# Kernel optimization log

Measured on AMD Instinct MI355X. Metric: run time of the kernel, lower is better.

The kernel has to match this reference:

```python
import jax, jax.numpy as jnp
import numpy as np

N_NODES = 100000
N_EDGES = 1600000
IN_DIM = 128
HID = 64
OUT_DIM = 3


def _glorot(key, shape):
    fan_in, fan_out = shape[0], shape[1]
    std = (2.0 / (fan_in + fan_out)) ** 0.5
    return jax.random.normal(key, shape, jnp.float32) * std


def setup_inputs() -> dict:
    key = jax.random.key(0)
    ks = jax.random.split(key, 12)
    x = jax.random.normal(ks[0], (N_NODES, IN_DIM), jnp.float32)
    edge_index = jax.random.randint(ks[1], (2, N_EDGES), 0, N_NODES, dtype=jnp.int32)
    return {
        "x": x,
        "edge_index": edge_index,
        "W1": _glorot(ks[2], (IN_DIM, HID)), "b1": jnp.zeros((HID,), jnp.float32),
        "W2": _glorot(ks[3], (HID, HID)), "b2": jnp.zeros((HID,), jnp.float32),
        "W3": _glorot(ks[4], (HID, HID)), "b3": jnp.zeros((HID,), jnp.float32),
        "W4": _glorot(ks[5], (HID, HID // 2)), "b4": jnp.zeros((HID // 2,), jnp.float32),
        "Wh": _glorot(ks[6], (HID // 2, OUT_DIM)), "bh": jnp.zeros((OUT_DIM,), jnp.float32),
    }


def reference(x, edge_index, W1, b1, W2, b2, W3, b3, W4, b4, Wh, bh):
    n = x.shape[0]
    self_loops = jnp.arange(n, dtype=edge_index.dtype)
    src = jnp.concatenate([edge_index[0], self_loops])  # message sources j
    dst = jnp.concatenate([edge_index[1], self_loops])  # aggregation targets i
    # symmetric GCN normalization with self-loops: deg over targets (unit edge weights)
    deg = jax.ops.segment_sum(jnp.ones_like(dst, jnp.float32), dst, num_segments=n)
    dinv = jnp.where(deg > 0, jax.lax.rsqrt(deg), 0.0)
    norm = dinv[src] * dinv[dst]  # [E+N]

    def gcn(h, W, b):
        h = h @ W  # transform first (PyG GCNConv order)
        agg = jax.ops.segment_sum(h[src] * norm[:, None], dst, num_segments=n)
        return agg + b

    h = jax.nn.relu(gcn(x, W1, b1))   # dropout is identity in eval mode
    h = jax.nn.relu(gcn(h, W2, b2))
    h = jax.nn.relu(gcn(h, W3, b3))
    h = jax.nn.relu(gcn(h, W4, b4))
    return h @ Wh + bh  # [N, 3]
```

## Files before the change

### kernel.cpp

```cpp
#include <hip/hip_runtime.h>
#include <hip/hip_bf16.h>
#include <hip/hip_fp16.h>
#include <cstdint>


#define MAXD 512
#define EB   8192

__global__ __launch_bounds__(256) void hist1_k(const int* __restrict__ ei,
                                               int* __restrict__ histM,
                                               int E, int ND) {
    __shared__ int hist[MAXD];
    const int tid = threadIdx.x, b = blockIdx.x;
    hist[tid] = 0; hist[tid + 256] = 0;
    __syncthreads();
    const int base = b * EB;
#pragma unroll 2
    for (int it = 0; it < EB / 256; it += 4) {
        int d[4]; bool ok[4];
#pragma unroll
        for (int u = 0; u < 4; ++u) {
            int e = base + (it + u) * 256 + tid;
            ok[u] = e < E;
            d[u] = ok[u] ? ei[E + e] : 0;
        }
#pragma unroll
        for (int u = 0; u < 4; ++u)
            if (ok[u]) atomicAdd(&hist[d[u] >> 8], 1);
    }
    __syncthreads();
    histM[(size_t)b * MAXD + tid] = hist[tid];
    histM[(size_t)b * MAXD + tid + 256] = hist[tid + 256];
}

__global__ __launch_bounds__(256) void scan_digits_k(int* __restrict__ histM,
                                                     int* __restrict__ totals,
                                                     int NBLK) {
    __shared__ int s[256];
    const int t = threadIdx.x, dg = blockIdx.x;
    int v = (t < NBLK) ? histM[(size_t)t * MAXD + dg] : 0;
    s[t] = v;
    __syncthreads();
    for (int off = 1; off < 256; off <<= 1) {
        int x = (t >= off) ? s[t - off] : 0;
        __syncthreads();
        s[t] += x;
        __syncthreads();
    }
    if (t < NBLK) histM[(size_t)t * MAXD + dg] = s[t] - v;
    if (t == 255) totals[dg] = s[255];
}

__global__ __launch_bounds__(512) void scan_base_k(const int* __restrict__ totals,
                                                   int* __restrict__ cb, int ND) {
    __shared__ int s[512];
    const int t = threadIdx.x;
    int v = (t < ND) ? totals[t] : 0;
    s[t] = v;
    __syncthreads();
    for (int off = 1; off < 512; off <<= 1) {
        int x = (t >= off) ? s[t - off] : 0;
        __syncthreads();
        s[t] += x;
        __syncthreads();
    }
    if (t < ND) cb[t] = s[t] - v;
    if (t == 511) cb[ND] = s[511];
}

template <int K, int OUT, bool HALF_OUT>
__device__ __forceinline__ void gemm_body(const float* __restrict__ H,
                                          const float* __restrict__ W,
                                          const float* __restrict__ dinv,
                                          void* __restrict__ Tout, int n, int bx) {
    constexpr int TX  = OUT / 4;
    constexpr int TY  = 256 / TX;
    constexpr int BM  = TY * 4;
    constexpr int BK  = 32;
    constexpr int PAD = 4;

    __shared__ float At[BK][BM + PAD];
    __shared__ float Ws[BK][OUT];

    const int t    = threadIdx.x;
    const int cx   = t % TX;
    const int ry   = t / TX;
    const int row0 = bx * BM;

    float acc[4][4] = {{0.f}};
    const int arow = t >> 3;
    const int af4  = t & 7;

    for (int k0 = 0; k0 < K; k0 += BK) {
#pragma unroll
        for (int p = 0; p < BM / 32; ++p) {
            int r  = arow + p * 32;
            int gr = row0 + r;
            int grc = gr < n ? gr : n - 1;
            float4 v = *reinterpret_cast<const float4*>(
                H + (size_t)grc * K + k0 + af4 * 4);
            At[af4 * 4 + 0][r] = v.x;
            At[af4 * 4 + 1][r] = v.y;
            At[af4 * 4 + 2][r] = v.z;
            At[af4 * 4 + 3][r] = v.w;
        }
#pragma unroll
        for (int p = 0; p < (BK * OUT) / 1024; ++p) {
            int idx = t + p * 256;
            int wk  = idx / (OUT / 4);
            int wf  = idx % (OUT / 4);
            float4 v = *reinterpret_cast<const float4*>(
                W + (size_t)(k0 + wk) * OUT + wf * 4);
            *reinterpret_cast<float4*>(&Ws[wk][wf * 4]) = v;
        }
        __syncthreads();
#pragma unroll
        for (int k = 0; k < BK; ++k) {
            float4 a = *reinterpret_cast<const float4*>(&At[k][ry * 4]);
            float4 w = *reinterpret_cast<const float4*>(&Ws[k][cx * 4]);
            acc[0][0] = fmaf(a.x, w.x, acc[0][0]);
            acc[0][1] = fmaf(a.x, w.y, acc[0][1]);
            acc[0][2] = fmaf(a.x, w.z, acc[0][2]);
            acc[0][3] = fmaf(a.x, w.w, acc[0][3]);
            acc[1][0] = fmaf(a.y, w.x, acc[1][0]);
            acc[1][1] = fmaf(a.y, w.y, acc[1][1]);
            acc[1][2] = fmaf(a.y, w.z, acc[1][2]);
            acc[1][3] = fmaf(a.y, w.w, acc[1][3]);
            acc[2][0] = fmaf(a.z, w.x, acc[2][0]);
            acc[2][1] = fmaf(a.z, w.y, acc[2][1]);
            acc[2][2] = fmaf(a.z, w.z, acc[2][2]);
            acc[2][3] = fmaf(a.z, w.w, acc[2][3]);
            acc[3][0] = fmaf(a.w, w.x, acc[3][0]);
            acc[3][1] = fmaf(a.w, w.y, acc[3][1]);
            acc[3][2] = fmaf(a.w, w.z, acc[3][2]);
            acc[3][3] = fmaf(a.w, w.w, acc[3][3]);
        }
        __syncthreads();
    }
#pragma unroll
    for (int i = 0; i < 4; ++i) {
        int gr = row0 + ry * 4 + i;
        if (gr < n) {
            if constexpr (HALF_OUT) {
                float di = dinv[gr];
                union { ushort4 u; __half h[4]; } pk;
                pk.h[0] = __float2half_rn(acc[i][0] * di);
                pk.h[1] = __float2half_rn(acc[i][1] * di);
                pk.h[2] = __float2half_rn(acc[i][2] * di);
                pk.h[3] = __float2half_rn(acc[i][3] * di);
                *reinterpret_cast<ushort4*>(
                    (__half*)Tout + (size_t)gr * OUT + cx * 4) = pk.u;
            } else {
                float4 v = make_float4(acc[i][0], acc[i][1], acc[i][2], acc[i][3]);
                *reinterpret_cast<float4*>(
                    (float*)Tout + (size_t)gr * OUT + cx * 4) = v;
            }
        }
    }
}

__device__ __forceinline__ void pack_body(const int* __restrict__ ei,
                                          const int* __restrict__ histM,
                                          const int* __restrict__ cb,
                                          int* __restrict__ packed,
                                          int E, int ND, int b) {
    __shared__ int cur[MAXD];
    const int tid = threadIdx.x;
    for (int t = tid; t < ND; t += 256)
        cur[t] = cb[t] + histM[(size_t)b * MAXD + t];
    __syncthreads();
    const int base = b * EB;
#pragma unroll 2
    for (int it = 0; it < EB / 256; it += 4) {
        int s[4], d[4]; bool ok[4];
#pragma unroll
        for (int u = 0; u < 4; ++u) {
            int e = base + (it + u) * 256 + tid;
            ok[u] = e < E;
            if (ok[u]) { s[u] = ei[e]; d[u] = ei[E + e]; }
        }
#pragma unroll
        for (int u = 0; u < 4; ++u) {
            if (ok[u]) {
                int pos = atomicAdd(&cur[d[u] >> 8], 1);
                packed[pos] = (s[u] << 8) | (d[u] & 255);
            }
        }
    }
}

__global__ __launch_bounds__(256) void pack_gemm1_k(
    const int* __restrict__ ei, const int* __restrict__ histM,
    const int* __restrict__ cb, int* __restrict__ packed,
    const float* __restrict__ x, const float* __restrict__ W1,
    float* __restrict__ T1, int n, int E, int ND, int G, int F) {
    const int bx = blockIdx.x;
    const int M  = (G < F) ? G : F;
    bool is_pack;
    int idx;
    if (bx < 2 * M) { is_pack = (bx & 1) == 0; idx = bx >> 1; }
    else            { idx = M + (bx - 2 * M); is_pack = (F > G); }
    if (is_pack) pack_body(ei, histM, cb, packed, E, ND, idx);
    else         gemm_body<128, 64, false>(x, W1, nullptr, T1, n, idx);
}

__global__ __launch_bounds__(256) void bucket_k(const int* __restrict__ packed,
                                                const int* __restrict__ cb,
                                                int* __restrict__ col,
                                                int* __restrict__ rowptr,
                                                int* __restrict__ counts,
                                                float* __restrict__ dinv,
                                                const float* __restrict__ Traw,
                                                __half* __restrict__ Th, int n) {
    __shared__ int   hist[256];
    __shared__ int   pref[256];
    __shared__ int   cur[256];
    __shared__ float dinv_l[256];

    const int tid  = threadIdx.x;
    const int dg   = blockIdx.x;
    const int base = cb[dg];
    const int m    = cb[dg + 1] - base;

    hist[tid] = 0;
    __syncthreads();
    for (int k0 = 0; k0 < m; k0 += 1024) {
        int v[4]; bool ok[4];
#pragma unroll
        for (int u = 0; u < 4; ++u) {
            int k = k0 + u * 256 + tid;
            ok[u] = k < m;
            v[u] = ok[u] ? packed[base + k] : 0;
        }
#pragma unroll
        for (int u = 0; u < 4; ++u)
            if (ok[u]) atomicAdd(&hist[v[u] & 255], 1);
    }
    __syncthreads();
    int deg = hist[tid];
    pref[tid] = deg;
    __syncthreads();
    for (int off = 1; off < 256; off <<= 1) {
        int x = (tid >= off) ? pref[tid - off] : 0;
        __syncthreads();
        pref[tid] += x;
        __syncthreads();
    }
    int excl = pref[tid] - deg;
    float di = rsqrtf((float)(deg + 1));
    dinv_l[tid] = di;
    cur[tid] = base + excl;
    const int d = dg * 256 + tid;
    if (d < n) {
        counts[d] = deg;
        dinv[d]   = di;
        rowptr[d] = base + excl;
    }
    __syncthreads();
    for (int k0 = 0; k0 < m; k0 += 1024) {
        int v[4]; bool ok[4];
#pragma unroll
        for (int u = 0; u < 4; ++u) {
            int k = k0 + u * 256 + tid;
            ok[u] = k < m;
            v[u] = ok[u] ? packed[base + k] : 0;
        }
#pragma unroll
        for (int u = 0; u < 4; ++u) {
            if (ok[u]) {
                int pos = atomicAdd(&cur[v[u] & 255], 1);
                col[pos] = v[u] >> 8;
            }
        }
    }
    const int r0 = dg * 256;
#pragma unroll 4
    for (int it = 0; it < 16; ++it) {
        int idx = it * 256 + tid;
        int rl  = idx >> 4;
        int r   = r0 + rl;
        if (r < n) {
            float4 v = reinterpret_cast<const float4*>(Traw)[(size_t)r * 16 + (idx & 15)];
            float dd = dinv_l[rl];
            union { ushort4 u; __half h[4]; } pk;
            pk.h[0] = __float2half_rn(v.x * dd);
            pk.h[1] = __float2half_rn(v.y * dd);
            pk.h[2] = __float2half_rn(v.z * dd);
            pk.h[3] = __float2half_rn(v.w * dd);
            reinterpret_cast<ushort4*>(Th)[(size_t)r * 16 + (idx & 15)] = pk.u;
        }
    }
}

template <int K, int OUT>
__global__ __launch_bounds__(256) void gemm_h_k(const float* __restrict__ H,
                                                const float* __restrict__ W,
                                                const float* __restrict__ dinv,
                                                __half* __restrict__ T, int n) {
    gemm_body<K, OUT, true>(H, W, dinv, T, n, blockIdx.x);
}

template <int WIDTH, bool FUSE_HEAD>
__global__ __launch_bounds__(256) void agg_k(const __half* __restrict__ T,
                                             const int* __restrict__ rowptr,
                                             const int* __restrict__ counts,
                                             const int* __restrict__ col,
                                             const float* __restrict__ dinv,
                                             const float* __restrict__ bias,
                                             float* __restrict__ O, int n,
                                             const float* __restrict__ Wh,
                                             const float* __restrict__ bh) {
    constexpr int LR  = WIDTH / 4;
    constexpr int NSW = 64 / LR;
    constexpr int U   = 16 / NSW;
    const int lane = threadIdx.x & 63;
    const int q    = lane % LR;
    const int sw   = lane / LR;
    const int i = (blockIdx.x * blockDim.x + threadIdx.x) >> 6;
    if (i >= n) return;

    const int start = rowptr[i];
    const int cnt   = counts[i];
    const uint2* __restrict__ T2 = reinterpret_cast<const uint2*>(T);

    float4 acc = make_float4(0.f, 0.f, 0.f, 0.f);
    for (int base = 0; base < cnt; base += 64) {
        const int m = min(64, cnt - base);
        int c_l = (lane < m) ? col[start + base + lane] : 0;
        for (int jg = 0; jg < m; jg += 16) {
            int cc[U]; uint2 v[U]; float wm[U];
#pragma unroll
            for (int u = 0; u < U; ++u) {
                int j  = jg + u * NSW + sw;
                int jc = j < m ? j : 0;
                cc[u] = __shfl(c_l, jc, 64);
                wm[u] = (j < m) ? 1.f : 0.f;
            }
#pragma unroll
            for (int u = 0; u < U; ++u) v[u] = T2[(size_t)cc[u] * LR + q];
#pragma unroll
            for (int u = 0; u < U; ++u) {
                const __half2* h2 = reinterpret_cast<const __half2*>(&v[u]);
                float2 f0 = __half22float2(h2[0]);
                float2 f1 = __half22float2(h2[1]);
                acc.x = fmaf(f0.x, wm[u], acc.x);
                acc.y = fmaf(f0.y, wm[u], acc.y);
                acc.z = fmaf(f1.x, wm[u], acc.z);
                acc.w = fmaf(f1.y, wm[u], acc.w);
            }
        }
    }
    if (sw == 0) {
        uint2 v = T2[(size_t)i * LR + q];
        const __half2* h2 = reinterpret_cast<const __half2*>(&v);
        float2 f0 = __half22float2(h2[0]);
        float2 f1 = __half22float2(h2[1]);
        acc.x += f0.x; acc.y += f0.y; acc.z += f1.x; acc.w += f1.y;
    }
#pragma unroll
    for (int off = LR; off < 64; off <<= 1) {
        acc.x += __shfl_xor(acc.x, off, 64);
        acc.y += __shfl_xor(acc.y, off, 64);
        acc.z += __shfl_xor(acc.z, off, 64);
        acc.w += __shfl_xor(acc.w, off, 64);
    }
    const float di = dinv[i];
    const float4 b4 = reinterpret_cast<const float4*>(bias)[q];
    float4 h;
    h.x = fmaxf(fmaf(di, acc.x, b4.x), 0.f);
    h.y = fmaxf(fmaf(di, acc.y, b4.y), 0.f);
    h.z = fmaxf(fmaf(di, acc.z, b4.z), 0.f);
    h.w = fmaxf(fmaf(di, acc.w, b4.w), 0.f);
    if constexpr (!FUSE_HEAD) {
        if (sw == 0)
            reinterpret_cast<float4*>(O + (size_t)i * WIDTH)[q] = h;
    } else {
        float p0 = h.x * Wh[(4 * q + 0) * 3 + 0];
        float p1 = h.x * Wh[(4 * q + 0) * 3 + 1];
        float p2 = h.x * Wh[(4 * q + 0) * 3 + 2];
        p0 = fmaf(h.y, Wh[(4 * q + 1) * 3 + 0], p0);
        p1 = fmaf(h.y, Wh[(4 * q + 1) * 3 + 1], p1);
        p2 = fmaf(h.y, Wh[(4 * q + 1) * 3 + 2], p2);
        p0 = fmaf(h.z, Wh[(4 * q + 2) * 3 + 0], p0);
        p1 = fmaf(h.z, Wh[(4 * q + 2) * 3 + 1], p1);
        p2 = fmaf(h.z, Wh[(4 * q + 2) * 3 + 2], p2);
        p0 = fmaf(h.w, Wh[(4 * q + 3) * 3 + 0], p0);
        p1 = fmaf(h.w, Wh[(4 * q + 3) * 3 + 1], p1);
        p2 = fmaf(h.w, Wh[(4 * q + 3) * 3 + 2], p2);
#pragma unroll
        for (int off = 1; off < LR; off <<= 1) {
            p0 += __shfl_xor(p0, off, 64);
            p1 += __shfl_xor(p1, off, 64);
            p2 += __shfl_xor(p2, off, 64);
        }
        if (lane == 0) {
            O[(size_t)i * 3 + 0] = p0 + bh[0];
            O[(size_t)i * 3 + 1] = p1 + bh[1];
            O[(size_t)i * 3 + 2] = p2 + bh[2];
        }
    }
}

extern "C" void kernel_launch(void* const* d_in, const int* in_sizes, int n_in,
                              void* d_out, int out_size, void* d_ws, size_t ws_size,
                              hipStream_t stream) {
    const float* x  = (const float*)d_in[0];
    const int*   ei = (const int*)d_in[1];
    const float* W1 = (const float*)d_in[2];
    const float* b1 = (const float*)d_in[3];
    const float* W2 = (const float*)d_in[4];
    const float* b2 = (const float*)d_in[5];
    const float* W3 = (const float*)d_in[6];
    const float* b3 = (const float*)d_in[7];
    const float* W4 = (const float*)d_in[8];
    const float* b4 = (const float*)d_in[9];
    const float* Wh = (const float*)d_in[10];
    const float* bh = (const float*)d_in[11];
    float* out = (float*)d_out;

    const int n = in_sizes[0] / 128;
    const int E = in_sizes[1] / 2;
    const int ND   = (n + 255) / 256;
    const int NBLK = (E + EB - 1) / EB;

    char* ws = (char*)d_ws;
    auto alloc = [&](size_t bytes) {
        char* p = ws;
        ws += (bytes + 255) & ~(size_t)255;
        return p;
    };
    int*    histM  = (int*)alloc((size_t)NBLK * MAXD * 4);
    int*    totals = (int*)alloc((size_t)MAXD * 4);
    int*    cbA    = (int*)alloc((size_t)(MAXD + 1) * 4);
    int*    packed = (int*)alloc((size_t)E * 4);
    int*    col    = (int*)alloc((size_t)E * 4);
    int*    rowptr = (int*)alloc((size_t)n * 4);
    int*    counts = (int*)alloc((size_t)n * 4);
    float*  dinv   = (float*)alloc((size_t)n * 4);
    float*  bufF   = (float*)alloc((size_t)n * 64 * 4);
    __half* bufH   = (__half*)alloc((size_t)n * 64 * 2);

    dim3 blk(256);
    const int G = (n + 63) / 64;
    const int agg_blocks = (n + 3) / 4;

    hist1_k<<<dim3(NBLK), blk, 0, stream>>>(ei, histM, E, ND);
    scan_digits_k<<<dim3(ND), blk, 0, stream>>>(histM, totals, NBLK);
    scan_base_k<<<dim3(1), dim3(512), 0, stream>>>(totals, cbA, ND);
    pack_gemm1_k<<<dim3(NBLK + G), blk, 0, stream>>>(ei, histM, cbA, packed,
                                                     x, W1, bufF, n, E, ND, G, NBLK);
    bucket_k<<<dim3(ND), blk, 0, stream>>>(packed, cbA, col, rowptr, counts,
                                           dinv, bufF, bufH, n);
    agg_k<64, false><<<dim3(agg_blocks), blk, 0, stream>>>(
        bufH, rowptr, counts, col, dinv, b1, bufF, n, nullptr, nullptr);
    gemm_h_k<64, 64><<<dim3(G), blk, 0, stream>>>(bufF, W2, dinv, bufH, n);
    agg_k<64, false><<<dim3(agg_blocks), blk, 0, stream>>>(
        bufH, rowptr, counts, col, dinv, b2, bufF, n, nullptr, nullptr);
    gemm_h_k<64, 64><<<dim3(G), blk, 0, stream>>>(bufF, W3, dinv, bufH, n);
    agg_k<64, false><<<dim3(agg_blocks), blk, 0, stream>>>(
        bufH, rowptr, counts, col, dinv, b3, bufF, n, nullptr, nullptr);
    gemm_h_k<64, 32><<<dim3((n + 127) / 128), blk, 0, stream>>>(bufF, W4, dinv, bufH, n);
    agg_k<32, true><<<dim3(agg_blocks), blk, 0, stream>>>(
        bufH, rowptr, counts, col, dinv, b4, out, n, Wh, bh);
}
```

Baseline: 402.0 us.

## Pad CSR rows with self-loop and dummy zero node, fuse histogram with GEMM1

Each CSR row is padded to a multiple of 16 entries, with the self-loop placed in the first slot and the rest pointing to a zero dummy node at index n. This removes the bounds masks, the weight multiplies and the separate self-loop pass from the aggregation inner loop. Layer-1 GEMM work is split: one third is fused with the histogram kernel and the rest with the pack kernel, which now handles 4 edge chunks per block. The T buffer keeps a 64-half row stride even for the 32-wide layer. In exchange, the col array carries extra padding entries that the aggregation loads and accumulates.

```diff
diff --git a/kernel.cpp b/kernel.cpp
--- a/kernel.cpp
+++ b/kernel.cpp
@@ -6,12 +6,13 @@
 
 #define MAXD 512
 #define EB   8192
-
-__global__ __launch_bounds__(256) void hist1_k(const int* __restrict__ ei,
-                                               int* __restrict__ histM,
-                                               int E, int ND) {
+#define CH   4
+#define PADSLACK 4096
+
+__device__ __forceinline__ void hist_body(const int* __restrict__ ei,
+                                          int* __restrict__ histM, int E, int b) {
     __shared__ int hist[MAXD];
-    const int tid = threadIdx.x, b = blockIdx.x;
+    const int tid = threadIdx.x;
     hist[tid] = 0; hist[tid + 256] = 0;
     __syncthreads();
     const int base = b * EB;
@@ -149,7 +150,7 @@
                 pk.h[2] = __float2half_rn(acc[i][2] * di);
                 pk.h[3] = __float2half_rn(acc[i][3] * di);
                 *reinterpret_cast<ushort4*>(
-                    (__half*)Tout + (size_t)gr * OUT + cx * 4) = pk.u;
+                    (__half*)Tout + (size_t)gr * 64 + cx * 4) = pk.u;
             } else {
                 float4 v = make_float4(acc[i][0], acc[i][1], acc[i][2], acc[i][3]);
                 *reinterpret_cast<float4*>(
@@ -167,11 +168,10 @@
     __shared__ int cur[MAXD];
     const int tid = threadIdx.x;
     for (int t = tid; t < ND; t += 256)
-        cur[t] = cb[t] + histM[(size_t)b * MAXD + t];
-    __syncthreads();
-    const int base = b * EB;
-#pragma unroll 2
-    for (int it = 0; it < EB / 256; it += 4) {
+        cur[t] = cb[t] + histM[(size_t)(b * CH) * MAXD + t];
+    __syncthreads();
+    const int base = b * (CH * EB);
+    for (int it = 0; it < (CH * EB) / 256; it += 4) {
         int s[4], d[4]; bool ok[4];
 #pragma unroll
         for (int u = 0; u < 4; ++u) {
@@ -189,19 +189,23 @@
     }
 }
 
+__global__ __launch_bounds__(256) void hist_gemm1_k(
+    const int* __restrict__ ei, int* __restrict__ histM, int E,
+    const float* __restrict__ x, const float* __restrict__ W1,
+    float* __restrict__ T1, int n, int NH) {
+    const int bx = blockIdx.x;
+    if (bx < NH) hist_body(ei, histM, E, bx);
+    else         gemm_body<128, 64, false>(x, W1, nullptr, T1, n, bx - NH);
+}
+
 __global__ __launch_bounds__(256) void pack_gemm1_k(
     const int* __restrict__ ei, const int* __restrict__ histM,
     const int* __restrict__ cb, int* __restrict__ packed,
     const float* __restrict__ x, const float* __restrict__ W1,
-    float* __restrict__ T1, int n, int E, int ND, int G, int F) {
+    float* __restrict__ T1, int n, int E, int ND, int NPB, int G1) {
     const int bx = blockIdx.x;
-    const int M  = (G < F) ? G : F;
-    bool is_pack;
-    int idx;
-    if (bx < 2 * M) { is_pack = (bx & 1) == 0; idx = bx >> 1; }
-    else            { idx = M + (bx - 2 * M); is_pack = (F > G); }
-    if (is_pack) pack_body(ei, histM, cb, packed, E, ND, idx);
-    else         gemm_body<128, 64, false>(x, W1, nullptr, T1, n, idx);
+    if (bx < NPB) pack_body(ei, histM, cb, packed, E, ND, bx);
+    else          gemm_body<128, 64, false>(x, W1, nullptr, T1, n, G1 + bx - NPB);
 }
 
 __global__ __launch_bounds__(256) void bucket_k(const int* __restrict__ packed,
@@ -217,10 +221,11 @@
     __shared__ int   cur[256];
     __shared__ float dinv_l[256];
 
-    const int tid  = threadIdx.x;
-    const int dg   = blockIdx.x;
-    const int base = cb[dg];
-    const int m    = cb[dg + 1] - base;
+    const int tid   = threadIdx.x;
+    const int dg    = blockIdx.x;
+    const int base  = cb[dg];
+    const int m     = cb[dg + 1] - base;
+    const int basep = base + dg * PADSLACK;
 
     hist[tid] = 0;
     __syncthreads();
@@ -237,8 +242,9 @@
             if (ok[u]) atomicAdd(&hist[v[u] & 255], 1);
     }
     __syncthreads();
-    int deg = hist[tid];
-    pref[tid] = deg;
+    const int deg   = hist[tid];
+    const int cnt_p = (deg + 16) & ~15;
+    pref[tid] = cnt_p;
     __syncthreads();
     for (int off = 1; off < 256; off <<= 1) {
         int x = (tid >= off) ? pref[tid - off] : 0;
@@ -246,15 +252,17 @@
         pref[tid] += x;
         __syncthreads();
     }
-    int excl = pref[tid] - deg;
-    float di = rsqrtf((float)(deg + 1));
+    const int rp = basep + pref[tid] - cnt_p;
+    const float di = rsqrtf((float)(deg + 1));
     dinv_l[tid] = di;
-    cur[tid] = base + excl;
+    cur[tid] = rp + 1;
     const int d = dg * 256 + tid;
     if (d < n) {
-        counts[d] = deg;
+        counts[d] = cnt_p;
         dinv[d]   = di;
-        rowptr[d] = base + excl;
+        rowptr[d] = rp;
+        col[rp]   = d;
+        for (int k = deg + 1; k < cnt_p; ++k) col[rp + k] = n;
     }
     __syncthreads();
     for (int k0 = 0; k0 < m; k0 += 1024) {
@@ -290,6 +298,10 @@
             reinterpret_cast<ushort4*>(Th)[(size_t)r * 16 + (idx & 15)] = pk.u;
         }
     }
+    if (dg == 0 && tid < 16) {
+        uint2 z; z.x = 0u; z.y = 0u;
+        reinterpret_cast<uint2*>(Th)[(size_t)n * 16 + tid] = z;
+    }
 }
 
 template <int K, int OUT>
@@ -300,7 +312,7 @@
     gemm_body<K, OUT, true>(H, W, dinv, T, n, blockIdx.x);
 }
 
-template <int WIDTH, bool FUSE_HEAD>
+template <int LR, bool FUSE_HEAD>
 __global__ __launch_bounds__(256) void agg_k(const __half* __restrict__ T,
                                              const int* __restrict__ rowptr,
                                              const int* __restrict__ counts,
@@ -310,7 +322,6 @@
                                              float* __restrict__ O, int n,
                                              const float* __restrict__ Wh,
                                              const float* __restrict__ bh) {
-    constexpr int LR  = WIDTH / 4;
     constexpr int NSW = 64 / LR;
     constexpr int U   = 16 / NSW;
     const int lane = threadIdx.x & 63;
@@ -326,36 +337,22 @@
     float4 acc = make_float4(0.f, 0.f, 0.f, 0.f);
     for (int base = 0; base < cnt; base += 64) {
         const int m = min(64, cnt - base);
-        int c_l = (lane < m) ? col[start + base + lane] : 0;
+        int c_l = col[start + base + lane];
         for (int jg = 0; jg < m; jg += 16) {
-            int cc[U]; uint2 v[U]; float wm[U];
-#pragma unroll
-            for (int u = 0; u < U; ++u) {
-                int j  = jg + u * NSW + sw;
-                int jc = j < m ? j : 0;
-                cc[u] = __shfl(c_l, jc, 64);
-                wm[u] = (j < m) ? 1.f : 0.f;
-            }
-#pragma unroll
-            for (int u = 0; u < U; ++u) v[u] = T2[(size_t)cc[u] * LR + q];
+            int cc[U]; uint2 v[U];
+#pragma unroll
+            for (int u = 0; u < U; ++u)
+                cc[u] = __shfl(c_l, jg + u * NSW + sw, 64);
+#pragma unroll
+            for (int u = 0; u < U; ++u) v[u] = T2[(size_t)cc[u] * 16 + q];
 #pragma unroll
             for (int u = 0; u < U; ++u) {
                 const __half2* h2 = reinterpret_cast<const __half2*>(&v[u]);
                 float2 f0 = __half22float2(h2[0]);
                 float2 f1 = __half22float2(h2[1]);
-                acc.x = fmaf(f0.x, wm[u], acc.x);
-                acc.y = fmaf(f0.y, wm[u], acc.y);
-                acc.z = fmaf(f1.x, wm[u], acc.z);
-                acc.w = fmaf(f1.y, wm[u], acc.w);
+                acc.x += f0.x; acc.y += f0.y; acc.z += f1.x; acc.w += f1.y;
             }
         }
-    }
-    if (sw == 0) {
-        uint2 v = T2[(size_t)i * LR + q];
-        const __half2* h2 = reinterpret_cast<const __half2*>(&v);
-        float2 f0 = __half22float2(h2[0]);
-        float2 f1 = __half22float2(h2[1]);
-        acc.x += f0.x; acc.y += f0.y; acc.z += f1.x; acc.w += f1.y;
     }
 #pragma unroll
     for (int off = LR; off < 64; off <<= 1) {
@@ -373,7 +370,7 @@
     h.w = fmaxf(fmaf(di, acc.w, b4.w), 0.f);
     if constexpr (!FUSE_HEAD) {
         if (sw == 0)
-            reinterpret_cast<float4*>(O + (size_t)i * WIDTH)[q] = h;
+            reinterpret_cast<float4*>(O + (size_t)i * 64)[q] = h;
     } else {
         float p0 = h.x * Wh[(4 * q + 0) * 3 + 0];
         float p1 = h.x * Wh[(4 * q + 0) * 3 + 1];
@@ -422,6 +419,7 @@
     const int E = in_sizes[1] / 2;
     const int ND   = (n + 255) / 256;
     const int NBLK = (E + EB - 1) / EB;
+    const int NPB  = (NBLK + CH - 1) / CH;
 
     char* ws = (char*)d_ws;
     auto alloc = [&](size_t bytes) {
@@ -433,33 +431,35 @@
     int*    totals = (int*)alloc((size_t)MAXD * 4);
     int*    cbA    = (int*)alloc((size_t)(MAXD + 1) * 4);
     int*    packed = (int*)alloc((size_t)E * 4);
-    int*    col    = (int*)alloc((size_t)E * 4);
+    int*    col    = (int*)alloc(((size_t)E + (size_t)ND * PADSLACK + 256) * 4);
     int*    rowptr = (int*)alloc((size_t)n * 4);
     int*    counts = (int*)alloc((size_t)n * 4);
     float*  dinv   = (float*)alloc((size_t)n * 4);
     float*  bufF   = (float*)alloc((size_t)n * 64 * 4);
-    __half* bufH   = (__half*)alloc((size_t)n * 64 * 2);
+    __half* bufH   = (__half*)alloc(((size_t)n + 1) * 64 * 2);
 
     dim3 blk(256);
-    const int G = (n + 63) / 64;
+    const int G  = (n + 63) / 64;
+    const int G1 = G / 3;
+    const int G2 = G - G1;
     const int agg_blocks = (n + 3) / 4;
 
-    hist1_k<<<dim3(NBLK), blk, 0, stream>>>(ei, histM, E, ND);
+    hist_gemm1_k<<<dim3(NBLK + G1), blk, 0, stream>>>(ei, histM, E, x, W1, bufF, n, NBLK);
     scan_digits_k<<<dim3(ND), blk, 0, stream>>>(histM, totals, NBLK);
     scan_base_k<<<dim3(1), dim3(512), 0, stream>>>(totals, cbA, ND);
-    pack_gemm1_k<<<dim3(NBLK + G), blk, 0, stream>>>(ei, histM, cbA, packed,
-                                                     x, W1, bufF, n, E, ND, G, NBLK);
+    pack_gemm1_k<<<dim3(NPB + G2), blk, 0, stream>>>(ei, histM, cbA, packed,
+                                                     x, W1, bufF, n, E, ND, NPB, G1);
     bucket_k<<<dim3(ND), blk, 0, stream>>>(packed, cbA, col, rowptr, counts,
                                            dinv, bufF, bufH, n);
-    agg_k<64, false><<<dim3(agg_blocks), blk, 0, stream>>>(
+    agg_k<16, false><<<dim3(agg_blocks), blk, 0, stream>>>(
         bufH, rowptr, counts, col, dinv, b1, bufF, n, nullptr, nullptr);
     gemm_h_k<64, 64><<<dim3(G), blk, 0, stream>>>(bufF, W2, dinv, bufH, n);
-    agg_k<64, false><<<dim3(agg_blocks), blk, 0, stream>>>(
+    agg_k<16, false><<<dim3(agg_blocks), blk, 0, stream>>>(
         bufH, rowptr, counts, col, dinv, b2, bufF, n, nullptr, nullptr);
     gemm_h_k<64, 64><<<dim3(G), blk, 0, stream>>>(bufF, W3, dinv, bufH, n);
-    agg_k<64, false><<<dim3(agg_blocks), blk, 0, stream>>>(
+    agg_k<16, false><<<dim3(agg_blocks), blk, 0, stream>>>(
         bufH, rowptr, counts, col, dinv, b3, bufF, n, nullptr, nullptr);
     gemm_h_k<64, 32><<<dim3((n + 127) / 128), blk, 0, stream>>>(bufF, W4, dinv, bufH, n);
-    agg_k<32, true><<<dim3(agg_blocks), blk, 0, stream>>>(
+    agg_k<8, true><<<dim3(agg_blocks), blk, 0, stream>>>(
         bufH, rowptr, counts, col, dinv, b4, out, n, Wh, bh);
 }
```

Result: no change. 400.3 us (-0.4%).
